# Kernel optimization log

Measured on AMD Instinct MI355X. Metric: run time of the kernel, lower is better.

## Reference

```python
import jax, jax.numpy as jnp
import numpy as np

TOP_K = 2

def setup_inputs() -> dict:
    key = jax.random.key(0)
    k1, k2, k3, k4, k5 = jax.random.split(key, 5)
    B, S, H, E, F = 2, 1024, 1024, 8, 2816
    scale = 0.02
    return {
        "hidden_states": jax.random.normal(k1, (B, S, H), dtype=jnp.float32),
        "gate_w": jax.random.normal(k2, (E, H), dtype=jnp.float32) * scale,
        "w1": jax.random.normal(k3, (E, H, F), dtype=jnp.float32) * scale,
        "w3": jax.random.normal(k4, (E, H, F), dtype=jnp.float32) * scale,
        "w2": jax.random.normal(k5, (E, F, H), dtype=jnp.float32) * scale,
    }

def reference(hidden_states, gate_w, w1, w3, w2):
    B, S, H = hidden_states.shape
    E = gate_w.shape[0]
    x = hidden_states.reshape(-1, H)                      # [T, H]
    T = x.shape[0]
    # Router: logits -> fp32 softmax -> top-k -> renormalize
    router_logits = jnp.einsum('th,eh->te', x, gate_w)    # [T, E]
    probs = jax.nn.softmax(router_logits.astype(jnp.float32), axis=-1)
    top_w, top_i = jax.lax.top_k(probs, TOP_K)            # [T, k]
    top_w = top_w / jnp.sum(top_w, axis=-1, keepdims=True)
    # Scatter normalized top-k weights into dense combine matrix [T, E]
    combine = jnp.zeros((T, E), dtype=probs.dtype)
    combine = combine.at[jnp.arange(T)[:, None], top_i].set(top_w)
    combine = combine.astype(x.dtype)
    # Experts: SwiGLU MLP per expert, weighted combine (dense formulation
    # of gather -> grouped GEMM -> scatter; non-selected experts get weight 0)
    g = jnp.einsum('th,ehf->tef', x, w1)                  # gate proj
    u = jnp.einsum('th,ehf->tef', x, w3)                  # up proj
    act = jax.nn.silu(g) * u                              # [T, E, F]
    act = act * combine[:, :, None]                       # apply routing weight
    out = jnp.einsum('tef,efh->th', act, w2)              # down proj + combine
    final_hidden_states = out.reshape(B, S, H)
    return final_hidden_states, router_logits
```

## Files before the change

### kernel.cpp

```cpp
#include <hip/hip_runtime.h>

typedef unsigned short u16;
typedef unsigned int u32;
typedef __attribute__((ext_vector_type(8))) short bf16x8;
typedef __attribute__((ext_vector_type(4))) float f32x4;

#define T_TOK 2048
#define H_DIM 1024
#define E_NUM 8
#define F_DIM 2816
#define BM 64
#define BN 64
#define BK 32

__device__ __forceinline__ u16 f2bf(float f) {
    u32 b = __float_as_uint(f);
    u32 lsb = (b >> 16) & 1u;
    b += 0x7fffu + lsb;
    return (u16)(b >> 16);
}

__global__ __launch_bounds__(64) void router_kernel(
    const float* __restrict__ x, const float* __restrict__ gw,
    float* __restrict__ logits_out, int* __restrict__ cnt,
    int* __restrict__ tok_list, float* __restrict__ wt_list)
{
    int t = blockIdx.x;
    int lane = threadIdx.x;
    const float* xr = x + (size_t)t * H_DIM;

    float acc[E_NUM];
#pragma unroll
    for (int e = 0; e < E_NUM; e++) acc[e] = 0.f;

    for (int j = 0; j < H_DIM / 64; j++) {
        int idx = j * 64 + lane;
        float xv = xr[idx];
#pragma unroll
        for (int e = 0; e < E_NUM; e++)
            acc[e] += xv * gw[e * H_DIM + idx];
    }
#pragma unroll
    for (int e = 0; e < E_NUM; e++) {
        float v = acc[e];
#pragma unroll
        for (int o = 32; o > 0; o >>= 1) v += __shfl_xor(v, o, 64);
        acc[e] = v;
    }
    if (lane == 0) {
#pragma unroll
        for (int e = 0; e < E_NUM; e++) logits_out[t * E_NUM + e] = acc[e];
        float m = acc[0];
#pragma unroll
        for (int e = 1; e < E_NUM; e++) m = fmaxf(m, acc[e]);
        float p[E_NUM], s = 0.f;
#pragma unroll
        for (int e = 0; e < E_NUM; e++) { p[e] = expf(acc[e] - m); s += p[e]; }
        float inv = 1.f / s;
#pragma unroll
        for (int e = 0; e < E_NUM; e++) p[e] *= inv;
        int i0 = 0;
#pragma unroll
        for (int e = 1; e < E_NUM; e++) if (p[e] > p[i0]) i0 = e;
        int i1 = (i0 == 0) ? 1 : 0;
#pragma unroll
        for (int e = 0; e < E_NUM; e++) if (e != i0 && p[e] > p[i1]) i1 = e;
        float w0 = p[i0], w1 = p[i1];
        float rs = 1.f / (w0 + w1);
        w0 *= rs; w1 *= rs;
        int s0 = atomicAdd(&cnt[i0], 1);
        tok_list[i0 * T_TOK + s0] = t; wt_list[i0 * T_TOK + s0] = w0;
        int s1 = atomicAdd(&cnt[i1], 1);
        tok_list[i1 * T_TOK + s1] = t; wt_list[i1 * T_TOK + s1] = w1;
    }
}

__global__ void offsets_kernel(const int* __restrict__ cnt, int* __restrict__ off)
{
    if (threadIdx.x == 0 && blockIdx.x == 0) {
        int s = 0;
        for (int e = 0; e < E_NUM; e++) {
            off[e] = s;
            s += ((cnt[e] + BM - 1) / BM) * BM;
        }
    }
}

__global__ __launch_bounds__(256) void gemm1_kernel(
    const float* __restrict__ x, const float* __restrict__ w1,
    const float* __restrict__ w3, const int* __restrict__ cnt,
    const int* __restrict__ off, const int* __restrict__ tok_list,
    const float* __restrict__ wt_list, u16* __restrict__ act)
{
    int e = blockIdx.z;
    int m0 = blockIdx.y * BM;
    int n0 = blockIdx.x * BN;
    int c = cnt[e];
    if (m0 >= c) return;

    __shared__ __align__(16) u16 As[BM][40];
    __shared__ __align__(16) u16 B1[BN][40];
    __shared__ __align__(16) u16 B3[BN][40];
    __shared__ int tok_s[BM];
    __shared__ float wt_s[BM];

    int tid = threadIdx.x;
    if (tid < BM) {
        int tok = tok_list[e * T_TOK + m0 + tid];
        tok_s[tid] = tok;
        wt_s[tid] = (tok >= 0) ? wt_list[e * T_TOK + m0 + tid] : 0.f;
    }
    __syncthreads();

    int w = tid >> 6, lane = tid & 63, q = lane >> 4, l15 = lane & 15;
    int wm = (w >> 1) * 32, wn = (w & 1) * 32;

    f32x4 zero = {0.f, 0.f, 0.f, 0.f};
    f32x4 accg[2][2], accu[2][2];
#pragma unroll
    for (int tm = 0; tm < 2; tm++)
#pragma unroll
        for (int tn = 0; tn < 2; tn++) { accg[tm][tn] = zero; accu[tm][tn] = zero; }

    int ar = tid >> 2, ac0 = (tid & 3) * 8;
    int bk = tid >> 3, bf0 = (tid & 7) * 8;
    int tokA = tok_s[ar];
    const size_t wbase = (size_t)e * H_DIM * F_DIM;

    for (int k0 = 0; k0 < H_DIM; k0 += BK) {
        float a8[8];
#pragma unroll
        for (int i = 0; i < 8; i++) a8[i] = 0.f;
        if (tokA >= 0) {
            float4 v0 = *(const float4*)(x + (size_t)tokA * H_DIM + k0 + ac0);
            float4 v1 = *(const float4*)(x + (size_t)tokA * H_DIM + k0 + ac0 + 4);
            a8[0] = v0.x; a8[1] = v0.y; a8[2] = v0.z; a8[3] = v0.w;
            a8[4] = v1.x; a8[5] = v1.y; a8[6] = v1.z; a8[7] = v1.w;
        }
        union { uint4 v; u16 u[8]; } au;
#pragma unroll
        for (int i = 0; i < 8; i++) au.u[i] = f2bf(a8[i]);
        *(uint4*)&As[ar][ac0] = au.v;

        const size_t boff = wbase + (size_t)(k0 + bk) * F_DIM + n0 + bf0;
        float4 b1a = *(const float4*)(w1 + boff);
        float4 b1b = *(const float4*)(w1 + boff + 4);
        float4 b3a = *(const float4*)(w3 + boff);
        float4 b3b = *(const float4*)(w3 + boff + 4);
        float b1v[8] = {b1a.x, b1a.y, b1a.z, b1a.w, b1b.x, b1b.y, b1b.z, b1b.w};
        float b3v[8] = {b3a.x, b3a.y, b3a.z, b3a.w, b3b.x, b3b.y, b3b.z, b3b.w};
#pragma unroll
        for (int i = 0; i < 8; i++) {
            B1[bf0 + i][bk] = f2bf(b1v[i]);
            B3[bf0 + i][bk] = f2bf(b3v[i]);
        }
        __syncthreads();

        bf16x8 a[2], b1f[2], b3f[2];
#pragma unroll
        for (int tm = 0; tm < 2; tm++)
            a[tm] = *(const bf16x8*)&As[wm + tm * 16 + l15][q * 8];
#pragma unroll
        for (int tn = 0; tn < 2; tn++) {
            b1f[tn] = *(const bf16x8*)&B1[wn + tn * 16 + l15][q * 8];
            b3f[tn] = *(const bf16x8*)&B3[wn + tn * 16 + l15][q * 8];
        }
#pragma unroll
        for (int tm = 0; tm < 2; tm++)
#pragma unroll
            for (int tn = 0; tn < 2; tn++) {
                accg[tm][tn] = __builtin_amdgcn_mfma_f32_16x16x32_bf16(a[tm], b1f[tn], accg[tm][tn], 0, 0, 0);
                accu[tm][tn] = __builtin_amdgcn_mfma_f32_16x16x32_bf16(a[tm], b3f[tn], accu[tm][tn], 0, 0, 0);
            }
        __syncthreads();
    }

    int pos0 = off[e] + m0;
#pragma unroll
    for (int tm = 0; tm < 2; tm++)
#pragma unroll
        for (int tn = 0; tn < 2; tn++)
#pragma unroll
            for (int r = 0; r < 4; r++) {
                int row = wm + tm * 16 + q * 4 + r;
                float g = accg[tm][tn][r];
                float u = accu[tm][tn][r];
                float wt = wt_s[row];
                float sg = g / (1.f + expf(-g));
                float val = sg * u * wt;
                int col = n0 + wn + tn * 16 + l15;
                act[(size_t)(pos0 + row) * F_DIM + col] = f2bf(val);
            }
}

__global__ __launch_bounds__(256) void gemm2_kernel(
    const u16* __restrict__ act, const float* __restrict__ w2,
    const int* __restrict__ cnt, const int* __restrict__ off,
    const int* __restrict__ tok_list, float* __restrict__ accum)
{
    int e = blockIdx.z;
    int m0 = blockIdx.y * BM;
    int n0 = blockIdx.x * BN;
    int c = cnt[e];
    if (m0 >= c) return;

    __shared__ __align__(16) u16 As[BM][40];
    __shared__ __align__(16) u16 Bt[BN][40];
    __shared__ int tok_s[BM];

    int tid = threadIdx.x;
    if (tid < BM) tok_s[tid] = tok_list[e * T_TOK + m0 + tid];
    __syncthreads();

    int w = tid >> 6, lane = tid & 63, q = lane >> 4, l15 = lane & 15;
    int wm = (w >> 1) * 32, wn = (w & 1) * 32;

    f32x4 zero = {0.f, 0.f, 0.f, 0.f};
    f32x4 acc[2][2];
#pragma unroll
    for (int tm = 0; tm < 2; tm++)
#pragma unroll
        for (int tn = 0; tn < 2; tn++) acc[tm][tn] = zero;

    int ar = tid >> 2, ac0 = (tid & 3) * 8;
    int bk = tid >> 3, bf0 = (tid & 7) * 8;
    const size_t arow = (size_t)(off[e] + m0 + ar) * F_DIM;
    const size_t wbase = (size_t)e * F_DIM * H_DIM;

    for (int k0 = 0; k0 < F_DIM; k0 += BK) {
        uint4 av = *(const uint4*)(act + arow + k0 + ac0);
        *(uint4*)&As[ar][ac0] = av;

        const size_t boff = wbase + (size_t)(k0 + bk) * H_DIM + n0 + bf0;
        float4 ba = *(const float4*)(w2 + boff);
        float4 bb = *(const float4*)(w2 + boff + 4);
        float bv[8] = {ba.x, ba.y, ba.z, ba.w, bb.x, bb.y, bb.z, bb.w};
#pragma unroll
        for (int i = 0; i < 8; i++) Bt[bf0 + i][bk] = f2bf(bv[i]);
        __syncthreads();

        bf16x8 a[2], b[2];
#pragma unroll
        for (int tm = 0; tm < 2; tm++)
            a[tm] = *(const bf16x8*)&As[wm + tm * 16 + l15][q * 8];
#pragma unroll
        for (int tn = 0; tn < 2; tn++)
            b[tn] = *(const bf16x8*)&Bt[wn + tn * 16 + l15][q * 8];
#pragma unroll
        for (int tm = 0; tm < 2; tm++)
#pragma unroll
            for (int tn = 0; tn < 2; tn++)
                acc[tm][tn] = __builtin_amdgcn_mfma_f32_16x16x32_bf16(a[tm], b[tn], acc[tm][tn], 0, 0, 0);
        __syncthreads();
    }

#pragma unroll
    for (int tm = 0; tm < 2; tm++)
#pragma unroll
        for (int tn = 0; tn < 2; tn++)
#pragma unroll
            for (int r = 0; r < 4; r++) {
                int row = wm + tm * 16 + q * 4 + r;
                int tok = tok_s[row];
                if (tok >= 0) {
                    int col = n0 + wn + tn * 16 + l15;
                    atomicAdd(&accum[(size_t)tok * H_DIM + col], acc[tm][tn][r]);
                }
            }
}

__global__ __launch_bounds__(256) void conv_kernel(
    const float* __restrict__ accum, float* __restrict__ out)
{
    int i = blockIdx.x * 256 + threadIdx.x;
    out[i] = accum[i];
}

extern "C" void kernel_launch(void* const* d_in, const int* in_sizes, int n_in,
                              void* d_out, int out_size, void* d_ws, size_t ws_size,
                              hipStream_t stream) {
    const float* x  = (const float*)d_in[0];
    const float* gw = (const float*)d_in[1];
    const float* w1 = (const float*)d_in[2];
    const float* w3 = (const float*)d_in[3];
    const float* w2 = (const float*)d_in[4];
    float* out = (float*)d_out;

    char* ws = (char*)d_ws;
    int*   cnt      = (int*)(ws);
    int*   off      = (int*)(ws + 64);
    int*   tok_list = (int*)(ws + 128);
    float* wt_list  = (float*)(ws + 128 + 65536);
    float* accum    = (float*)(ws + 128 + 131072);
    u16*   act      = (u16*)(ws + 128 + 131072 + 8388608);

    hipMemsetAsync(cnt, 0, 64, stream);
    hipMemsetAsync(tok_list, 0xFF, 65536, stream);
    hipMemsetAsync(accum, 0, (size_t)T_TOK * H_DIM * 4, stream);

    float* logits_out = out + (size_t)T_TOK * H_DIM;
    router_kernel<<<T_TOK, 64, 0, stream>>>(x, gw, logits_out, cnt, tok_list, wt_list);
    offsets_kernel<<<1, 64, 0, stream>>>(cnt, off);
    gemm1_kernel<<<dim3(F_DIM / BN, T_TOK / BM, E_NUM), 256, 0, stream>>>(
        x, w1, w3, cnt, off, tok_list, wt_list, act);
    gemm2_kernel<<<dim3(H_DIM / BN, T_TOK / BM, E_NUM), 256, 0, stream>>>(
        act, w2, cnt, off, tok_list, accum);
    conv_kernel<<<(T_TOK * H_DIM) / 256, 256, 0, stream>>>(accum, out);
}
```

Measured before the change: 691.8 us.

## Persist expert GEMM blocks over M tiles to reuse weights and drop accum buffer

Restructures both expert GEMMs so each block owns an N tile of one expert and loops over all token tiles, with BM raised to 128. Weight loads are made coalesced across lanes and converted with a cheaper packed bf16 rounding. The fp32 accumulate buffer and copy kernel are removed by atomically adding straight into the output. This cuts repeated weight traffic at the cost of far fewer blocks and serialized tile loops.

```diff
diff --git a/kernel.cpp b/kernel.cpp
--- a/kernel.cpp
+++ b/kernel.cpp
@@ -9,15 +9,23 @@
 #define H_DIM 1024
 #define E_NUM 8
 #define F_DIM 2816
-#define BM 64
+#define BM 128
 #define BN 64
 #define BK 32
-
+#define LDK 40
+#define MAX_SLOTS 5120
+
+__device__ __forceinline__ u32 pkbf(float hi, float lo) {
+    u32 a = __float_as_uint(hi) + 0x8000u;
+    u32 b = __float_as_uint(lo) + 0x8000u;
+#if __has_builtin(__builtin_amdgcn_perm)
+    return __builtin_amdgcn_perm(a, b, 0x07060302u);
+#else
+    return (a & 0xFFFF0000u) | (b >> 16);
+#endif
+}
 __device__ __forceinline__ u16 f2bf(float f) {
-    u32 b = __float_as_uint(f);
-    u32 lsb = (b >> 16) & 1u;
-    b += 0x7fffu + lsb;
-    return (u16)(b >> 16);
+    return (u16)((__float_as_uint(f) + 0x8000u) >> 16);
 }
 
 __global__ __launch_bounds__(64) void router_kernel(
@@ -83,197 +91,216 @@
             off[e] = s;
             s += ((cnt[e] + BM - 1) / BM) * BM;
         }
-    }
-}
-
-__global__ __launch_bounds__(256) void gemm1_kernel(
+        off[E_NUM] = s;
+    }
+}
+
+__global__ __launch_bounds__(256, 2) void gemm1_kernel(
     const float* __restrict__ x, const float* __restrict__ w1,
     const float* __restrict__ w3, const int* __restrict__ cnt,
     const int* __restrict__ off, const int* __restrict__ tok_list,
     const float* __restrict__ wt_list, u16* __restrict__ act)
 {
-    int e = blockIdx.z;
-    int m0 = blockIdx.y * BM;
+    int e = blockIdx.y;
     int n0 = blockIdx.x * BN;
     int c = cnt[e];
-    if (m0 >= c) return;
-
-    __shared__ __align__(16) u16 As[BM][40];
-    __shared__ __align__(16) u16 B1[BN][40];
-    __shared__ __align__(16) u16 B3[BN][40];
+    int nmt = (c + BM - 1) / BM;
+    int base_slot = off[e];
+
+    __shared__ __align__(16) u16 As[BM][LDK];
+    __shared__ __align__(16) u16 B1s[BN][LDK];
+    __shared__ __align__(16) u16 B3s[BN][LDK];
     __shared__ int tok_s[BM];
     __shared__ float wt_s[BM];
 
     int tid = threadIdx.x;
-    if (tid < BM) {
-        int tok = tok_list[e * T_TOK + m0 + tid];
-        tok_s[tid] = tok;
-        wt_s[tid] = (tok >= 0) ? wt_list[e * T_TOK + m0 + tid] : 0.f;
-    }
-    __syncthreads();
-
     int w = tid >> 6, lane = tid & 63, q = lane >> 4, l15 = lane & 15;
-    int wm = (w >> 1) * 32, wn = (w & 1) * 32;
-
-    f32x4 zero = {0.f, 0.f, 0.f, 0.f};
-    f32x4 accg[2][2], accu[2][2];
-#pragma unroll
-    for (int tm = 0; tm < 2; tm++)
-#pragma unroll
-        for (int tn = 0; tn < 2; tn++) { accg[tm][tn] = zero; accu[tm][tn] = zero; }
-
-    int ar = tid >> 2, ac0 = (tid & 3) * 8;
-    int bk = tid >> 3, bf0 = (tid & 7) * 8;
-    int tokA = tok_s[ar];
-    const size_t wbase = (size_t)e * H_DIM * F_DIM;
-
-    for (int k0 = 0; k0 < H_DIM; k0 += BK) {
-        float a8[8];
-#pragma unroll
-        for (int i = 0; i < 8; i++) a8[i] = 0.f;
-        if (tokA >= 0) {
-            float4 v0 = *(const float4*)(x + (size_t)tokA * H_DIM + k0 + ac0);
-            float4 v1 = *(const float4*)(x + (size_t)tokA * H_DIM + k0 + ac0 + 4);
-            a8[0] = v0.x; a8[1] = v0.y; a8[2] = v0.z; a8[3] = v0.w;
-            a8[4] = v1.x; a8[5] = v1.y; a8[6] = v1.z; a8[7] = v1.w;
-        }
-        union { uint4 v; u16 u[8]; } au;
-#pragma unroll
-        for (int i = 0; i < 8; i++) au.u[i] = f2bf(a8[i]);
-        *(uint4*)&As[ar][ac0] = au.v;
-
-        const size_t boff = wbase + (size_t)(k0 + bk) * F_DIM + n0 + bf0;
-        float4 b1a = *(const float4*)(w1 + boff);
-        float4 b1b = *(const float4*)(w1 + boff + 4);
-        float4 b3a = *(const float4*)(w3 + boff);
-        float4 b3b = *(const float4*)(w3 + boff + 4);
-        float b1v[8] = {b1a.x, b1a.y, b1a.z, b1a.w, b1b.x, b1b.y, b1b.z, b1b.w};
-        float b3v[8] = {b3a.x, b3a.y, b3a.z, b3a.w, b3b.x, b3b.y, b3b.z, b3b.w};
-#pragma unroll
-        for (int i = 0; i < 8; i++) {
-            B1[bf0 + i][bk] = f2bf(b1v[i]);
-            B3[bf0 + i][bk] = f2bf(b3v[i]);
+    int wm = (w >> 1) * 64, wn = (w & 1) * 32;
+    int arow = tid >> 1, koff = (tid & 1) * 16;
+    int bn = lane, kseg = (tid >> 6) * 8;
+
+    const size_t wofs = (size_t)e * H_DIM * F_DIM + n0 + bn;
+    const float* w1p = w1 + wofs;
+    const float* w3p = w3 + wofs;
+
+    for (int mt = 0; mt < nmt; ++mt) {
+        __syncthreads();
+        if (tid < BM) {
+            int tk = tok_list[e * T_TOK + mt * BM + tid];
+            tok_s[tid] = tk;
+            wt_s[tid] = (tk >= 0) ? wt_list[e * T_TOK + mt * BM + tid] : 0.f;
         }
         __syncthreads();
-
-        bf16x8 a[2], b1f[2], b3f[2];
-#pragma unroll
-        for (int tm = 0; tm < 2; tm++)
-            a[tm] = *(const bf16x8*)&As[wm + tm * 16 + l15][q * 8];
-#pragma unroll
-        for (int tn = 0; tn < 2; tn++) {
-            b1f[tn] = *(const bf16x8*)&B1[wn + tn * 16 + l15][q * 8];
-            b3f[tn] = *(const bf16x8*)&B3[wn + tn * 16 + l15][q * 8];
+        int tokA = tok_s[arow];
+        const float* xa = x + (size_t)(tokA < 0 ? 0 : tokA) * H_DIM + koff;
+
+        f32x4 zero = {0.f, 0.f, 0.f, 0.f};
+        f32x4 accg[4][2], accu[4][2];
+#pragma unroll
+        for (int tm = 0; tm < 4; tm++)
+#pragma unroll
+            for (int tn = 0; tn < 2; tn++) { accg[tm][tn] = zero; accu[tm][tn] = zero; }
+
+        for (int k0 = 0; k0 < H_DIM; k0 += BK) {
+            uint4 qa0 = {0u,0u,0u,0u}, qa1 = {0u,0u,0u,0u};
+            if (tokA >= 0) {
+                const float4* p = (const float4*)(xa + k0);
+                float4 f0 = p[0], f1 = p[1], f2 = p[2], f3 = p[3];
+                qa0.x = pkbf(f0.y, f0.x); qa0.y = pkbf(f0.w, f0.z);
+                qa0.z = pkbf(f1.y, f1.x); qa0.w = pkbf(f1.w, f1.z);
+                qa1.x = pkbf(f2.y, f2.x); qa1.y = pkbf(f2.w, f2.z);
+                qa1.z = pkbf(f3.y, f3.x); qa1.w = pkbf(f3.w, f3.z);
+            }
+            *(uint4*)&As[arow][koff] = qa0;
+            *(uint4*)&As[arow][koff + 8] = qa1;
+
+            {
+                const float* bp = w1p + (size_t)(k0 + kseg) * F_DIM;
+                float c0 = bp[0];          float c1 = bp[(size_t)F_DIM];
+                float c2 = bp[2*(size_t)F_DIM]; float c3 = bp[3*(size_t)F_DIM];
+                float c4 = bp[4*(size_t)F_DIM]; float c5 = bp[5*(size_t)F_DIM];
+                float c6 = bp[6*(size_t)F_DIM]; float c7 = bp[7*(size_t)F_DIM];
+                uint4 qb;
+                qb.x = pkbf(c1, c0); qb.y = pkbf(c3, c2);
+                qb.z = pkbf(c5, c4); qb.w = pkbf(c7, c6);
+                *(uint4*)&B1s[bn][kseg] = qb;
+            }
+            {
+                const float* bp = w3p + (size_t)(k0 + kseg) * F_DIM;
+                float c0 = bp[0];          float c1 = bp[(size_t)F_DIM];
+                float c2 = bp[2*(size_t)F_DIM]; float c3 = bp[3*(size_t)F_DIM];
+                float c4 = bp[4*(size_t)F_DIM]; float c5 = bp[5*(size_t)F_DIM];
+                float c6 = bp[6*(size_t)F_DIM]; float c7 = bp[7*(size_t)F_DIM];
+                uint4 qb;
+                qb.x = pkbf(c1, c0); qb.y = pkbf(c3, c2);
+                qb.z = pkbf(c5, c4); qb.w = pkbf(c7, c6);
+                *(uint4*)&B3s[bn][kseg] = qb;
+            }
+            __syncthreads();
+
+            bf16x8 a[4], bb1[2], bb3[2];
+#pragma unroll
+            for (int tm = 0; tm < 4; tm++)
+                a[tm] = *(const bf16x8*)&As[wm + tm * 16 + l15][q * 8];
+#pragma unroll
+            for (int tn = 0; tn < 2; tn++) {
+                bb1[tn] = *(const bf16x8*)&B1s[wn + tn * 16 + l15][q * 8];
+                bb3[tn] = *(const bf16x8*)&B3s[wn + tn * 16 + l15][q * 8];
+            }
+#pragma unroll
+            for (int tm = 0; tm < 4; tm++)
+#pragma unroll
+                for (int tn = 0; tn < 2; tn++) {
+                    accg[tm][tn] = __builtin_amdgcn_mfma_f32_16x16x32_bf16(a[tm], bb1[tn], accg[tm][tn], 0, 0, 0);
+                    accu[tm][tn] = __builtin_amdgcn_mfma_f32_16x16x32_bf16(a[tm], bb3[tn], accu[tm][tn], 0, 0, 0);
+                }
+            __syncthreads();
         }
-#pragma unroll
-        for (int tm = 0; tm < 2; tm++)
+
+        int srow = base_slot + mt * BM;
+#pragma unroll
+        for (int tm = 0; tm < 4; tm++)
 #pragma unroll
             for (int tn = 0; tn < 2; tn++) {
-                accg[tm][tn] = __builtin_amdgcn_mfma_f32_16x16x32_bf16(a[tm], b1f[tn], accg[tm][tn], 0, 0, 0);
-                accu[tm][tn] = __builtin_amdgcn_mfma_f32_16x16x32_bf16(a[tm], b3f[tn], accu[tm][tn], 0, 0, 0);
-            }
-        __syncthreads();
-    }
-
-    int pos0 = off[e] + m0;
-#pragma unroll
-    for (int tm = 0; tm < 2; tm++)
-#pragma unroll
-        for (int tn = 0; tn < 2; tn++)
-#pragma unroll
-            for (int r = 0; r < 4; r++) {
-                int row = wm + tm * 16 + q * 4 + r;
-                float g = accg[tm][tn][r];
-                float u = accu[tm][tn][r];
-                float wt = wt_s[row];
-                float sg = g / (1.f + expf(-g));
-                float val = sg * u * wt;
                 int col = n0 + wn + tn * 16 + l15;
-                act[(size_t)(pos0 + row) * F_DIM + col] = f2bf(val);
-            }
-}
-
-__global__ __launch_bounds__(256) void gemm2_kernel(
+#pragma unroll
+                for (int r = 0; r < 4; r++) {
+                    int row = wm + tm * 16 + q * 4 + r;
+                    float g = accg[tm][tn][r];
+                    float u = accu[tm][tn][r];
+                    float wt = wt_s[row];
+                    float val = (g / (1.f + __expf(-g))) * u * wt;
+                    act[(size_t)(srow + row) * F_DIM + col] = f2bf(val);
+                }
+            }
+    }
+}
+
+__global__ __launch_bounds__(256, 2) void gemm2_kernel(
     const u16* __restrict__ act, const float* __restrict__ w2,
     const int* __restrict__ cnt, const int* __restrict__ off,
-    const int* __restrict__ tok_list, float* __restrict__ accum)
+    const int* __restrict__ tok_list, float* __restrict__ outp)
 {
     int e = blockIdx.z;
-    int m0 = blockIdx.y * BM;
+    int half = blockIdx.y;
     int n0 = blockIdx.x * BN;
     int c = cnt[e];
-    if (m0 >= c) return;
-
-    __shared__ __align__(16) u16 As[BM][40];
-    __shared__ __align__(16) u16 Bt[BN][40];
+    int nmt = (c + BM - 1) / BM;
+    int base_slot = off[e];
+
+    __shared__ __align__(16) u16 As[BM][LDK];
+    __shared__ __align__(16) u16 Bt[BN][LDK];
     __shared__ int tok_s[BM];
 
     int tid = threadIdx.x;
-    if (tid < BM) tok_s[tid] = tok_list[e * T_TOK + m0 + tid];
-    __syncthreads();
-
     int w = tid >> 6, lane = tid & 63, q = lane >> 4, l15 = lane & 15;
-    int wm = (w >> 1) * 32, wn = (w & 1) * 32;
-
-    f32x4 zero = {0.f, 0.f, 0.f, 0.f};
-    f32x4 acc[2][2];
-#pragma unroll
-    for (int tm = 0; tm < 2; tm++)
-#pragma unroll
-        for (int tn = 0; tn < 2; tn++) acc[tm][tn] = zero;
-
-    int ar = tid >> 2, ac0 = (tid & 3) * 8;
-    int bk = tid >> 3, bf0 = (tid & 7) * 8;
-    const size_t arow = (size_t)(off[e] + m0 + ar) * F_DIM;
-    const size_t wbase = (size_t)e * F_DIM * H_DIM;
-
-    for (int k0 = 0; k0 < F_DIM; k0 += BK) {
-        uint4 av = *(const uint4*)(act + arow + k0 + ac0);
-        *(uint4*)&As[ar][ac0] = av;
-
-        const size_t boff = wbase + (size_t)(k0 + bk) * H_DIM + n0 + bf0;
-        float4 ba = *(const float4*)(w2 + boff);
-        float4 bb = *(const float4*)(w2 + boff + 4);
-        float bv[8] = {ba.x, ba.y, ba.z, ba.w, bb.x, bb.y, bb.z, bb.w};
-#pragma unroll
-        for (int i = 0; i < 8; i++) Bt[bf0 + i][bk] = f2bf(bv[i]);
+    int wm = (w >> 1) * 64, wn = (w & 1) * 32;
+    int arow = tid >> 1, koff = (tid & 1) * 16;
+    int bn = lane, kseg = (tid >> 6) * 8;
+
+    const float* w2p = w2 + (size_t)e * F_DIM * H_DIM + n0 + bn;
+
+    for (int mt = half; mt < nmt; mt += 2) {
         __syncthreads();
-
-        bf16x8 a[2], b[2];
-#pragma unroll
-        for (int tm = 0; tm < 2; tm++)
-            a[tm] = *(const bf16x8*)&As[wm + tm * 16 + l15][q * 8];
-#pragma unroll
-        for (int tn = 0; tn < 2; tn++)
-            b[tn] = *(const bf16x8*)&Bt[wn + tn * 16 + l15][q * 8];
-#pragma unroll
-        for (int tm = 0; tm < 2; tm++)
+        if (tid < BM) tok_s[tid] = tok_list[e * T_TOK + mt * BM + tid];
+        __syncthreads();
+
+        f32x4 zero = {0.f, 0.f, 0.f, 0.f};
+        f32x4 acc[4][2];
+#pragma unroll
+        for (int tm = 0; tm < 4; tm++)
+#pragma unroll
+            for (int tn = 0; tn < 2; tn++) acc[tm][tn] = zero;
+
+        int srow = base_slot + mt * BM;
+        const u16* ap = act + (size_t)(srow + arow) * F_DIM + koff;
+
+        for (int k0 = 0; k0 < F_DIM; k0 += BK) {
+            uint4 qa0 = *(const uint4*)(ap + k0);
+            uint4 qa1 = *(const uint4*)(ap + k0 + 8);
+            *(uint4*)&As[arow][koff] = qa0;
+            *(uint4*)&As[arow][koff + 8] = qa1;
+
+            const float* bp = w2p + (size_t)(k0 + kseg) * H_DIM;
+            float c0 = bp[0];            float c1 = bp[H_DIM];
+            float c2 = bp[2*H_DIM];      float c3 = bp[3*H_DIM];
+            float c4 = bp[4*H_DIM];      float c5 = bp[5*H_DIM];
+            float c6 = bp[6*H_DIM];      float c7 = bp[7*H_DIM];
+            uint4 qb;
+            qb.x = pkbf(c1, c0); qb.y = pkbf(c3, c2);
+            qb.z = pkbf(c5, c4); qb.w = pkbf(c7, c6);
+            *(uint4*)&Bt[bn][kseg] = qb;
+            __syncthreads();
+
+            bf16x8 a[4], b[2];
+#pragma unroll
+            for (int tm = 0; tm < 4; tm++)
+                a[tm] = *(const bf16x8*)&As[wm + tm * 16 + l15][q * 8];
 #pragma unroll
             for (int tn = 0; tn < 2; tn++)
-                acc[tm][tn] = __builtin_amdgcn_mfma_f32_16x16x32_bf16(a[tm], b[tn], acc[tm][tn], 0, 0, 0);
-        __syncthreads();
-    }
-
-#pragma unroll
-    for (int tm = 0; tm < 2; tm++)
-#pragma unroll
-        for (int tn = 0; tn < 2; tn++)
-#pragma unroll
-            for (int r = 0; r < 4; r++) {
-                int row = wm + tm * 16 + q * 4 + r;
-                int tok = tok_s[row];
-                if (tok >= 0) {
-                    int col = n0 + wn + tn * 16 + l15;
-                    atomicAdd(&accum[(size_t)tok * H_DIM + col], acc[tm][tn][r]);
+                b[tn] = *(const bf16x8*)&Bt[wn + tn * 16 + l15][q * 8];
+#pragma unroll
+            for (int tm = 0; tm < 4; tm++)
+#pragma unroll
+                for (int tn = 0; tn < 2; tn++)
+                    acc[tm][tn] = __builtin_amdgcn_mfma_f32_16x16x32_bf16(a[tm], b[tn], acc[tm][tn], 0, 0, 0);
+            __syncthreads();
+        }
+
+#pragma unroll
+        for (int tm = 0; tm < 4; tm++)
+#pragma unroll
+            for (int tn = 0; tn < 2; tn++) {
+                int col = n0 + wn + tn * 16 + l15;
+#pragma unroll
+                for (int r = 0; r < 4; r++) {
+                    int row = wm + tm * 16 + q * 4 + r;
+                    int tok = tok_s[row];
+                    if (tok >= 0)
+                        atomicAdd(&outp[(size_t)tok * H_DIM + col], acc[tm][tn][r]);
                 }
             }
-}
-
-__global__ __launch_bounds__(256) void conv_kernel(
-    const float* __restrict__ accum, float* __restrict__ out)
-{
-    int i = blockIdx.x * 256 + threadIdx.x;
-    out[i] = accum[i];
+    }
 }
 
 extern "C" void kernel_launch(void* const* d_in, const int* in_sizes, int n_in,
@@ -291,19 +318,17 @@
     int*   off      = (int*)(ws + 64);
     int*   tok_list = (int*)(ws + 128);
     float* wt_list  = (float*)(ws + 128 + 65536);
-    float* accum    = (float*)(ws + 128 + 131072);
-    u16*   act      = (u16*)(ws + 128 + 131072 + 8388608);
+    u16*   act      = (u16*)(ws + 131200);
 
     hipMemsetAsync(cnt, 0, 64, stream);
-    hipMemsetAsync(tok_list, 0xFF, 65536, stream);
-    hipMemsetAsync(accum, 0, (size_t)T_TOK * H_DIM * 4, stream);
+    hipMemsetAsync(tok_list, 0xFF, E_NUM * T_TOK * sizeof(int), stream);
+    hipMemsetAsync(out, 0, (size_t)T_TOK * H_DIM * sizeof(float), stream);
 
     float* logits_out = out + (size_t)T_TOK * H_DIM;
     router_kernel<<<T_TOK, 64, 0, stream>>>(x, gw, logits_out, cnt, tok_list, wt_list);
     offsets_kernel<<<1, 64, 0, stream>>>(cnt, off);
-    gemm1_kernel<<<dim3(F_DIM / BN, T_TOK / BM, E_NUM), 256, 0, stream>>>(
+    gemm1_kernel<<<dim3(F_DIM / BN, E_NUM), 256, 0, stream>>>(
         x, w1, w3, cnt, off, tok_list, wt_list, act);
-    gemm2_kernel<<<dim3(H_DIM / BN, T_TOK / BM, E_NUM), 256, 0, stream>>>(
-        act, w2, cnt, off, tok_list, accum);
-    conv_kernel<<<(T_TOK * H_DIM) / 256, 256, 0, stream>>>(accum, out);
-}
+    gemm2_kernel<<<dim3(H_DIM / BN, 2, E_NUM), 256, 0, stream>>>(
+        act, w2, cnt, off, tok_list, out);
+}
```

Measured after the change: 728.7 us. 1.05x slower.
